# Optimization experiments

Hardware: AMD Instinct MI355X
Metric: run time of the kernel (lower is better)

## Reference

```python
import jax, jax.numpy as jnp
import numpy as np

DIM = 2048
N_HEADS = 16
HEAD_DIM = DIM // N_HEADS
ROPE_BASE = 10000.0


def _rope_cos_sin(seq_len, head_dim, dtype):
    inv_freq = 1.0 / (ROPE_BASE ** (jnp.arange(0, head_dim, 2, dtype=jnp.float32) / head_dim))
    t = jnp.arange(seq_len, dtype=jnp.float32)
    freqs = jnp.einsum('s,d->sd', t, inv_freq)          # (S, hd/2)
    emb = jnp.concatenate([freqs, freqs], axis=-1)       # (S, hd)
    return jnp.cos(emb).astype(dtype), jnp.sin(emb).astype(dtype)


def _rotate_half(x):
    x1, x2 = jnp.split(x, 2, axis=-1)
    return jnp.concatenate([-x2, x1], axis=-1)


def _apply_rope(x, cos, sin):
    # x: (B, H, S, hd); cos/sin: (S, hd)
    return x * cos[None, None] + _rotate_half(x) * sin[None, None]


def setup_inputs() -> dict:
    key = jax.random.key(0)
    ks = jax.random.split(key, 5)
    B, S = 2, 2048
    scale = 1.0 / np.sqrt(DIM)
    return {
        'x': jax.random.normal(ks[0], (B, S, DIM), dtype=jnp.float32),
        'Wq': jax.random.normal(ks[1], (DIM, DIM), dtype=jnp.float32) * scale,
        'Wk': jax.random.normal(ks[2], (DIM, DIM), dtype=jnp.float32) * scale,
        'Wv': jax.random.normal(ks[3], (DIM, DIM), dtype=jnp.float32) * scale,
        'Wo': jax.random.normal(ks[4], (DIM, DIM), dtype=jnp.float32) * scale,
    }


def reference(x, Wq, Wk, Wv, Wo):
    B, S, _ = x.shape
    scale = HEAD_DIM ** -0.5

    def proj(W):
        # torch Linear: x @ W.T ; reshape to (B, H, S, hd)
        return (x @ W.T).reshape(B, S, N_HEADS, HEAD_DIM).transpose(0, 2, 1, 3)

    q, k, v = proj(Wq), proj(Wk), proj(Wv)
    cos, sin = _rope_cos_sin(S, HEAD_DIM, x.dtype)
    q = _apply_rope(q, cos, sin)
    k = _apply_rope(k, cos, sin)

    scores = jnp.einsum('bhqd,bhkd->bhqk', q, k) * scale  # (B,H,S,S)
    causal = jnp.triu(jnp.ones((S, S), dtype=bool), k=1)
    scores = jnp.where(causal[None, None], -jnp.inf, scores)
    attn = jax.nn.softmax(scores.astype(jnp.float32), axis=-1).astype(q.dtype)
    out = jnp.einsum('bhqk,bhkd->bhqd', attn, v)          # (B,H,S,hd)
    out = out.transpose(0, 2, 1, 3).reshape(B, S, DIM)
    return out @ Wo.T
```

## Files before the change

kernel.cpp:

```cpp
#include <hip/hip_runtime.h>


#define SEQ 2048
#define DMODEL 2048
#define NH 16
#define HD 128

typedef __attribute__((ext_vector_type(8))) short bf16x8;
typedef __attribute__((ext_vector_type(4))) float f32x4;

__device__ __forceinline__ unsigned short f2bf(float f) {
  unsigned int u = __float_as_uint(f);
  u += 0x7fffu + ((u >> 16) & 1u);
  return (unsigned short)(u >> 16);
}

__device__ __forceinline__ void g2l16(const void* g, void* l) {
  __builtin_amdgcn_global_load_lds((const __attribute__((address_space(1))) void*)g,
                                   (__attribute__((address_space(3))) void*)l,
                                   16, 0, 0);
}

__device__ __forceinline__ f32x4 mfma16(bf16x8 a, bf16x8 b, f32x4 c) {
  return __builtin_amdgcn_mfma_f32_16x16x32_bf16(a, b, c, 0, 0, 0);
}

template <int CTRL>
__device__ __forceinline__ float dpp_ror(float v) {
  return __int_as_float(__builtin_amdgcn_mov_dpp(__float_as_int(v), CTRL, 0xf, 0xf, false));
}
__device__ __forceinline__ float red_max16(float v) {
  v = fmaxf(v, dpp_ror<0x128>(v));
  v = fmaxf(v, dpp_ror<0x124>(v));
  v = fmaxf(v, dpp_ror<0x122>(v));
  v = fmaxf(v, dpp_ror<0x121>(v));
  return v;
}
__device__ __forceinline__ float red_sum16(float v) {
  v += dpp_ror<0x128>(v);
  v += dpp_ror<0x124>(v);
  v += dpp_ror<0x122>(v);
  v += dpp_ror<0x121>(v);
  return v;
}

__global__ __launch_bounds__(256) void cvt_all(const float* __restrict__ x,
                                               const float* __restrict__ wq,
                                               const float* __restrict__ wk,
                                               const float* __restrict__ wv,
                                               const float* __restrict__ wo,
                                               unsigned short* __restrict__ dst0,
                                               float2* __restrict__ rtab) {
  const int b = blockIdx.x;
  if (b >= 24576) {
    const int idx = (b - 24576) * 256 + threadIdx.x;
    const int s = idx >> 6, d = idx & 63;
    float sn, cs;
    sincosf((float)s * exp2f(-0.20762050593046f * (float)d), &sn, &cs);
    rtab[idx] = make_float2(cs, sn);
    return;
  }
  const float* src;
  unsigned short* dst;
  int idx, r = -1;
  if (b < 8192) {
    src = x; dst = dst0; idx = b * 256 + threadIdx.x;
  } else {
    r = (b - 8192) >> 12;
    src = (r == 0) ? wq : (r == 1) ? wk : (r == 2) ? wv : wo;
    dst = dst0 + (size_t)2 * SEQ * DMODEL + (size_t)r * DMODEL * DMODEL;
    idx = ((b - 8192) & 4095) * 256 + threadIdx.x;
  }
  const float4 v = ((const float4*)src)[idx];
  ushort4 o;
  o.x = f2bf(v.x); o.y = f2bf(v.y); o.z = f2bf(v.z); o.w = f2bf(v.w);
  int widx = idx;
  if (r == 0 || r == 1) {
    const int row = idx >> 9, col = idx & 511;
    const int o_ = row & 127;
    const int e = (((o_ >> 4) & 3) << 5) | (((o_ >> 6) & 1) << 4) | (o_ & 15);
    widx = (((row & ~127) | e) << 9) | col;
  }
  ((ushort4*)dst)[widx] = o;
}

template <int MODE>
__global__ __launch_bounds__(512, 2) void gemm_pipe(
    const unsigned short* __restrict__ A,
    const unsigned short* __restrict__ B,
    unsigned short* __restrict__ obf,
    float* __restrict__ of32,
    const float2* __restrict__ rtab) {
  constexpr int BN = (MODE == 0) ? 192 : 128;
  constexpr int NTW = BN / 32;
  constexpr int TILE = (256 + BN) * 64;
  constexpr int NU = 32 + BN / 8;
  constexpr int UPW = NU / 8;
  __shared__ unsigned short lds[2 * TILE];
  const int nb = blockIdx.x, mb = blockIdx.y;
  const int M0 = mb * 256;
  const int t = threadIdx.x;
  const int w = t >> 6, lane = t & 63, l15 = lane & 15, quad = lane >> 4;
  const int g = lane >> 3, j = lane & 7;
  const int wm = w >> 1, wn = w & 1;

  const unsigned short* Abase = A + (size_t)M0 * DMODEL;
  const unsigned short* Bbase = B + (size_t)nb * BN * DMODEL;

  f32x4 acc[4][NTW] = {};

  auto stage = [&](int buf, int k0, int i0, int i1) {
#pragma unroll
    for (int i = i0; i < i1; ++i) {
      const int u = w * UPW + i;
      if (u < 32) {
        g2l16(Abase + (size_t)(u * 8 + g) * DMODEL + k0 + ((j ^ g) << 3),
              &lds[buf * TILE + u * 512]);
      } else {
        g2l16(Bbase + (size_t)((u - 32) * 8 + g) * DMODEL + k0 + ((j ^ g) << 3),
              &lds[buf * TILE + 16384 + (u - 32) * 512]);
      }
    }
  };

  auto comp = [&](int buf, int kc) {
    const int c = kc * 4 + quad;
    const unsigned short* As_ = &lds[buf * TILE];
    const unsigned short* Bs_ = &lds[buf * TILE + 16384];
    bf16x8 af[4], bv[NTW];
#pragma unroll
    for (int mt = 0; mt < 4; ++mt) {
      const int m = wm * 64 + mt * 16 + l15;
      af[mt] = *(const bf16x8*)&As_[m * 64 + ((c ^ (m & 7)) << 3)];
    }
#pragma unroll
    for (int nt = 0; nt < NTW; ++nt) {
      const int n = wn * (BN / 2) + nt * 16 + l15;
      bv[nt] = *(const bf16x8*)&Bs_[n * 64 + ((c ^ (n & 7)) << 3)];
    }
#pragma unroll
    for (int nt = 0; nt < NTW; ++nt)
#pragma unroll
      for (int mt = 0; mt < 4; ++mt)
        acc[mt][nt] = mfma16(af[mt], bv[nt], acc[mt][nt]);
  };

  stage(0, 0, 0, UPW);
  asm volatile("s_waitcnt vmcnt(0)\n\ts_barrier" ::: "memory");

  int buf = 0;
  for (int tt = 0; tt < 32; ++tt) {
    const bool ps = (tt < 31);
    if (ps) stage(buf ^ 1, tt * 64 + 64, 0, UPW / 2);
    comp(buf, 0);
    if (ps) stage(buf ^ 1, tt * 64 + 64, UPW / 2, UPW);
    comp(buf, 1);
    if (ps) {
      asm volatile("s_waitcnt vmcnt(0)\n\ts_barrier" ::: "memory");
      buf ^= 1;
    }
  }

  if (MODE == 0) {
    const size_t NX = (size_t)2 * SEQ * DMODEL;
#pragma unroll
    for (int pp = 0; pp < NTW / 2; ++pp) {
      const int colb = nb * BN + wn * (BN / 2) + pp * 32;
      const int z = colb >> 11;
      const int zc = colb & 2047;
      const int h = zc >> 7;
      const int e0 = zc & 127;
      if (z < 2) {
        const float qscale = (z == 0) ? 0.1275174356f : 1.0f;
        unsigned short* O = obf + (size_t)z * NX;
        const int rt = (e0 >> 5) * 16 + l15;
#pragma unroll
        for (int mt = 0; mt < 4; ++mt)
#pragma unroll
          for (int reg = 0; reg < 4; ++reg) {
            const int m = M0 + wm * 64 + mt * 16 + quad * 4 + reg;
            const int bb = m >> 11, s = m & 2047;
            unsigned short* ob = O + ((size_t)(bb * NH + h) * SEQ + s) * HD;
            const float2 cs = rtab[s * 64 + rt];
            const float x1 = acc[mt][2 * pp][reg], x2 = acc[mt][2 * pp + 1][reg];
            ob[e0 + l15] = f2bf((x1 * cs.x - x2 * cs.y) * qscale);
            ob[e0 + 16 + l15] = f2bf((x2 * cs.x + x1 * cs.y) * qscale);
          }
      } else {
        unsigned short* Vb0 = obf + 2 * NX + (size_t)h * HD * SEQ;
#pragma unroll
        for (int q2 = 0; q2 < 2; ++q2) {
          const int d = e0 + q2 * 16 + l15;
#pragma unroll
          for (int mt = 0; mt < 4; ++mt)
#pragma unroll
            for (int reg = 0; reg < 4; ++reg) {
              const int m = M0 + wm * 64 + mt * 16 + quad * 4 + reg;
              const int bb = m >> 11, s = m & 2047;
              const int spos = (s & ~63) |
                               ((mt >> 1) * 32 + quad * 8 + reg * 2 + (mt & 1));
              unsigned short* ob = Vb0 + (size_t)bb * NH * HD * SEQ;
              ob[(size_t)d * SEQ + spos] = f2bf(acc[mt][2 * pp + q2][reg]);
            }
        }
      }
    }
  } else {
#pragma unroll
    for (int mt = 0; mt < 4; ++mt)
#pragma unroll
      for (int reg = 0; reg < 4; ++reg) {
        const int m = M0 + wm * 64 + mt * 16 + quad * 4 + reg;
#pragma unroll
        for (int nt = 0; nt < NTW; ++nt)
          of32[(size_t)m * DMODEL + nb * BN + wn * (BN / 2) + nt * 16 + l15] =
              acc[mt][nt][reg];
      }
  }
}

__global__ __launch_bounds__(512, 4) void attn_kernel(const unsigned short* __restrict__ Q,
                                                      const unsigned short* __restrict__ K,
                                                      const unsigned short* __restrict__ Vt,
                                                      unsigned short* __restrict__ Oa) {
  __shared__ unsigned short Ks[2][64 * 128];
  __shared__ unsigned short Vs[2][128 * 64];
  __shared__ unsigned short Ps[8][1024];
  const int gid = blockIdx.x;
  const int bh = gid & 31;
  const int qt = 15 - (gid >> 5);
  const unsigned short* Qb = Q + (size_t)bh * SEQ * HD;
  const unsigned short* Kb = K + (size_t)bh * SEQ * HD;
  const unsigned short* Vb = Vt + (size_t)bh * HD * SEQ;
  const int t = threadIdx.x;
  const int w = t >> 6, lane = t & 63, l15 = lane & 15, quad = lane >> 4;
  const int b = bh >> 4, h = bh & 15;

  auto stage = [&](int sb, int kt) {
    const unsigned short* Kt = Kb + (size_t)(kt * 64) * HD;
    const unsigned short* Vtk = Vb + kt * 64;
#pragma unroll
    for (int i = 0; i < 2; ++i) {
      const int u = i * 512 + t;
      const int key = u >> 4, cs = u & 15;
      g2l16(Kt + (size_t)key * HD + ((cs ^ (key & 7)) << 3),
            &Ks[sb][(i * 512 + w * 64) * 8]);
    }
#pragma unroll
    for (int i = 0; i < 2; ++i) {
      const int u = i * 512 + t;
      const int d = u >> 3, cs = u & 7;
      g2l16(Vtk + (size_t)d * SEQ + ((cs ^ (d & 7)) << 3),
            &Vs[sb][(i * 512 + w * 64) * 8]);
    }
  };

  bf16x8 qf[4];
#pragma unroll
  for (int ch = 0; ch < 4; ++ch)
    qf[ch] = *(const bf16x8*)(Qb + (size_t)(qt * 128 + w * 16 + l15) * HD +
                              ch * 32 + quad * 8);

  f32x4 o[8] = {};
  float mrow[4], lrow[4];
#pragma unroll
  for (int reg = 0; reg < 4; ++reg) { mrow[reg] = -1e30f; lrow[reg] = 0.f; }

  const int ktmax = 2 * qt + 1;
  stage(0, 0);
  asm volatile("s_waitcnt vmcnt(0)\n\ts_barrier" ::: "memory");
  int buf = 0;

  for (int kt = 0; kt <= ktmax; ++kt) {
    if (kt < ktmax) stage(buf ^ 1, kt + 1);

    const int ntm_raw = (qt * 128 + w * 16 + 15 - kt * 64) >> 4;
    const int ntm = ntm_raw > 3 ? 3 : ntm_raw;
    if (ntm >= 0) {
      f32x4 s[4] = {};
      __builtin_amdgcn_s_setprio(1);
#pragma unroll
      for (int ch = 0; ch < 4; ++ch) {
        const int c = ch * 4 + quad;
#pragma unroll
        for (int nt = 0; nt < 4; ++nt) {
          if (nt <= ntm) {
            const int n = nt * 16 + l15;
            const bf16x8 bv = *(const bf16x8*)&Ks[buf][n * 128 + ((c ^ (n & 7)) << 3)];
            s[nt] = mfma16(qf[ch], bv, s[nt]);
          }
        }
      }
      __builtin_amdgcn_s_setprio(0);

      if (kt >= 2 * qt) {
#pragma unroll
        for (int nt = 0; nt < 4; ++nt)
#pragma unroll
          for (int reg = 0; reg < 4; ++reg) {
            const int rr = qt * 128 + w * 16 + quad * 4 + reg;
            const int cc = kt * 64 + nt * 16 + l15;
            if (cc > rr) s[nt][reg] = -1e30f;
          }
      }

#pragma unroll
      for (int reg = 0; reg < 4; ++reg) {
        float vmax = fmaxf(fmaxf(s[0][reg], s[1][reg]), fmaxf(s[2][reg], s[3][reg]));
        vmax = red_max16(vmax);
        const float mo = mrow[reg];
        float mn = mo;
        if (!__all(vmax <= mo + 8.0f)) {
          mn = fmaxf(mo, vmax);
          const float alpha = exp2f(mo - mn);
          mrow[reg] = mn;
          lrow[reg] *= alpha;
#pragma unroll
          for (int nt = 0; nt < 8; ++nt) o[nt][reg] *= alpha;
        }
        float rs = 0.f;
#pragma unroll
        for (int nt = 0; nt < 4; ++nt) {
          const float p_ = exp2f(s[nt][reg] - mn);
          s[nt][reg] = p_;
          rs += p_;
        }
        rs = red_sum16(rs);
        lrow[reg] += rs;
      }

      unsigned short* Pw = Ps[w];
#pragma unroll
      for (int np = 0; np < 2; ++np)
#pragma unroll
        for (int reg = 0; reg < 4; ++reg) {
          unsigned int u;
          asm("v_cvt_pk_bf16_f32 %0, %1, %2"
              : "=v"(u)
              : "v"(s[np * 2][reg]), "v"(s[np * 2 + 1][reg]));
          const int r = quad * 4 + reg;
          const int ph = ((np ^ (quad & 1)) * 4 + (l15 >> 2) + r) & 7;
          *(unsigned int*)&Pw[r * 64 + ph * 8 + (l15 & 3) * 2] = u;
        }
      asm volatile("" ::: "memory");

      const int ch2max = (ntm >= 2) ? 1 : 0;
      __builtin_amdgcn_s_setprio(1);
#pragma unroll
      for (int ch2 = 0; ch2 < 2; ++ch2) {
        if (ch2 <= ch2max) {
          const int pnp = ch2 ^ ((l15 >> 2) & 1);
          const int ph = (pnp * 4 + quad + l15) & 7;
          const bf16x8 pa = *(const bf16x8*)&Pw[l15 * 64 + ph * 8];
          const int c = ch2 * 4 + quad;
#pragma unroll
          for (int nt = 0; nt < 8; ++nt) {
            const int d = nt * 16 + l15;
            const bf16x8 vv = *(const bf16x8*)&Vs[buf][d * 64 + ((c ^ (d & 7)) << 3)];
            o[nt] = mfma16(pa, vv, o[nt]);
          }
        }
      }
      __builtin_amdgcn_s_setprio(0);
    }

    asm volatile("s_waitcnt vmcnt(0)\n\ts_barrier" ::: "memory");
    buf ^= 1;
  }

#pragma unroll
  for (int reg = 0; reg < 4; ++reg) {
    const int sq = qt * 128 + w * 16 + quad * 4 + reg;
    const float inv_l = 1.0f / lrow[reg];
    unsigned short* ob = Oa + (size_t)(b * SEQ + sq) * DMODEL + h * HD;
#pragma unroll
    for (int nt = 0; nt < 8; ++nt) ob[nt * 16 + l15] = f2bf(o[nt][reg] * inv_l);
  }
}

extern "C" void kernel_launch(void* const* d_in, const int* in_sizes, int n_in,
                              void* d_out, int out_size, void* d_ws, size_t ws_size,
                              hipStream_t stream) {
  const float* x = (const float*)d_in[0];
  const float* Wq = (const float*)d_in[1];
  const float* Wk = (const float*)d_in[2];
  const float* Wv = (const float*)d_in[3];
  const float* Wo = (const float*)d_in[4];
  float* out = (float*)d_out;

  const size_t NX = (size_t)2 * SEQ * DMODEL;
  const size_t NW = (size_t)DMODEL * DMODEL;
  unsigned short* ws = (unsigned short*)d_ws;
  unsigned short* xb = ws;
  unsigned short* wqb = xb + NX;
  unsigned short* wkb = wqb + NW;
  unsigned short* wvb = wkb + NW;
  unsigned short* wob = wvb + NW;
  unsigned short* qb = wob + NW;
  unsigned short* kb = qb + NX;
  unsigned short* vb = kb + NX;
  unsigned short* ab = vb + NX;
  float2* rtab = (float2*)(ab + NX);

  cvt_all<<<25088, 256, 0, stream>>>(x, Wq, Wk, Wv, Wo, ws, rtab);
  gemm_pipe<0><<<dim3(32, 16), 512, 0, stream>>>(xb, wqb, qb, nullptr, rtab);
  attn_kernel<<<512, 512, 0, stream>>>(qb, kb, vb, ab);
  gemm_pipe<1><<<dim3(16, 16), 512, 0, stream>>>(ab, wob, nullptr, out, nullptr);
}
```

Baseline: 362.7 us.

## Shrink attention tiles to 64 queries x 32 keys with balanced causal scheduling

The attention kernel now uses 256-thread blocks that each handle 64 query rows, with 32-key K/V tiles instead of 64, and launches twice as many blocks. Query tiles are assigned in a zig-zag order across four rounds so the causal workload is spread more evenly. Staging pointers are precomputed and advanced each step, and the P and V LDS swizzles are redesigned for the 32-wide tile. The cost is more online-softmax rescale and barrier steps per unit of work, and less reuse of each K/V tile.

```diff
diff --git a/kernel.cpp b/kernel.cpp
--- a/kernel.cpp
+++ b/kernel.cpp
@@ -219,46 +219,48 @@
   }
 }
 
-__global__ __launch_bounds__(512, 4) void attn_kernel(const unsigned short* __restrict__ Q,
+__global__ __launch_bounds__(256, 4) void attn_kernel(const unsigned short* __restrict__ Q,
                                                       const unsigned short* __restrict__ K,
                                                       const unsigned short* __restrict__ Vt,
                                                       unsigned short* __restrict__ Oa) {
-  __shared__ unsigned short Ks[2][64 * 128];
-  __shared__ unsigned short Vs[2][128 * 64];
-  __shared__ unsigned short Ps[8][1024];
+  __shared__ unsigned short Ks[2][32 * 128];
+  __shared__ unsigned short Vs[2][128 * 32];
+  __shared__ unsigned short Ps[4][512];
   const int gid = blockIdx.x;
-  const int bh = gid & 31;
-  const int qt = 15 - (gid >> 5);
+  const int r = gid >> 8, c = gid & 255;
+  const int bh = c & 31, u = c >> 5;
+  const int qt = (r == 0) ? 31 - u : (r == 1) ? u : (r == 2) ? 23 - u : 8 + u;
   const unsigned short* Qb = Q + (size_t)bh * SEQ * HD;
-  const unsigned short* Kb = K + (size_t)bh * SEQ * HD;
-  const unsigned short* Vb = Vt + (size_t)bh * HD * SEQ;
   const int t = threadIdx.x;
   const int w = t >> 6, lane = t & 63, l15 = lane & 15, quad = lane >> 4;
   const int b = bh >> 4, h = bh & 15;
 
-  auto stage = [&](int sb, int kt) {
-    const unsigned short* Kt = Kb + (size_t)(kt * 64) * HD;
-    const unsigned short* Vtk = Vb + kt * 64;
-#pragma unroll
-    for (int i = 0; i < 2; ++i) {
-      const int u = i * 512 + t;
-      const int key = u >> 4, cs = u & 15;
-      g2l16(Kt + (size_t)key * HD + ((cs ^ (key & 7)) << 3),
-            &Ks[sb][(i * 512 + w * 64) * 8]);
-    }
-#pragma unroll
-    for (int i = 0; i < 2; ++i) {
-      const int u = i * 512 + t;
-      const int d = u >> 3, cs = u & 7;
-      g2l16(Vtk + (size_t)d * SEQ + ((cs ^ (d & 7)) << 3),
-            &Vs[sb][(i * 512 + w * 64) * 8]);
-    }
+  const int uk0 = t, uk1 = 256 + t;
+  const int k0key = uk0 >> 4, k0cs = uk0 & 15;
+  const int k1key = uk1 >> 4, k1cs = uk1 & 15;
+  const unsigned short* kp0 = K + (size_t)bh * SEQ * HD +
+                              (size_t)k0key * HD + (((k0cs ^ (k0key & 7)) & 15) << 3);
+  const unsigned short* kp1 = K + (size_t)bh * SEQ * HD +
+                              (size_t)k1key * HD + (((k1cs ^ (k1key & 7)) & 15) << 3);
+  const int v0d = uk0 >> 2, v0cs = uk0 & 3;
+  const int v1d = uk1 >> 2, v1cs = uk1 & 3;
+  const unsigned short* vp0 = Vt + (size_t)bh * HD * SEQ +
+                              (size_t)v0d * SEQ + ((v0cs ^ ((v0d >> 1) & 3)) << 3);
+  const unsigned short* vp1 = Vt + (size_t)bh * HD * SEQ +
+                              (size_t)v1d * SEQ + ((v1cs ^ ((v1d >> 1) & 3)) << 3);
+
+  auto stage = [&](int sb) {
+    g2l16(kp0, &Ks[sb][(w * 64) * 8]);
+    g2l16(kp1, &Ks[sb][(256 + w * 64) * 8]);
+    g2l16(vp0, &Vs[sb][(w * 64) * 8]);
+    g2l16(vp1, &Vs[sb][(256 + w * 64) * 8]);
+    kp0 += 32 * HD; kp1 += 32 * HD; vp0 += 32; vp1 += 32;
   };
 
   bf16x8 qf[4];
 #pragma unroll
   for (int ch = 0; ch < 4; ++ch)
-    qf[ch] = *(const bf16x8*)(Qb + (size_t)(qt * 128 + w * 16 + l15) * HD +
+    qf[ch] = *(const bf16x8*)(Qb + (size_t)(qt * 64 + w * 16 + l15) * HD +
                               ch * 32 + quad * 8);
 
   f32x4 o[8] = {};
@@ -267,46 +269,46 @@
   for (int reg = 0; reg < 4; ++reg) { mrow[reg] = -1e30f; lrow[reg] = 0.f; }
 
   const int ktmax = 2 * qt + 1;
-  stage(0, 0);
+  stage(0);
   asm volatile("s_waitcnt vmcnt(0)\n\ts_barrier" ::: "memory");
   int buf = 0;
 
   for (int kt = 0; kt <= ktmax; ++kt) {
-    if (kt < ktmax) stage(buf ^ 1, kt + 1);
-
-    const int ntm_raw = (qt * 128 + w * 16 + 15 - kt * 64) >> 4;
-    const int ntm = ntm_raw > 3 ? 3 : ntm_raw;
+    if (kt < ktmax) stage(buf ^ 1);
+
+    const bool dz = (kt >= 2 * qt);
+    const int ntm = dz ? ((qt * 64 + w * 16 + 15 - kt * 32) >> 4) : 1;
     if (ntm >= 0) {
-      f32x4 s[4] = {};
+      f32x4 s[2] = {};
       __builtin_amdgcn_s_setprio(1);
 #pragma unroll
       for (int ch = 0; ch < 4; ++ch) {
-        const int c = ch * 4 + quad;
-#pragma unroll
-        for (int nt = 0; nt < 4; ++nt) {
+        const int cc = ch * 4 + quad;
+#pragma unroll
+        for (int nt = 0; nt < 2; ++nt) {
           if (nt <= ntm) {
             const int n = nt * 16 + l15;
-            const bf16x8 bv = *(const bf16x8*)&Ks[buf][n * 128 + ((c ^ (n & 7)) << 3)];
+            const bf16x8 bv = *(const bf16x8*)&Ks[buf][n * 128 + ((cc ^ (n & 7)) << 3)];
             s[nt] = mfma16(qf[ch], bv, s[nt]);
           }
         }
       }
       __builtin_amdgcn_s_setprio(0);
 
-      if (kt >= 2 * qt) {
-#pragma unroll
-        for (int nt = 0; nt < 4; ++nt)
+      if (dz) {
+#pragma unroll
+        for (int nt = 0; nt < 2; ++nt)
 #pragma unroll
           for (int reg = 0; reg < 4; ++reg) {
-            const int rr = qt * 128 + w * 16 + quad * 4 + reg;
-            const int cc = kt * 64 + nt * 16 + l15;
+            const int rr = qt * 64 + w * 16 + quad * 4 + reg;
+            const int cc = kt * 32 + nt * 16 + l15;
             if (cc > rr) s[nt][reg] = -1e30f;
           }
       }
 
 #pragma unroll
       for (int reg = 0; reg < 4; ++reg) {
-        float vmax = fmaxf(fmaxf(s[0][reg], s[1][reg]), fmaxf(s[2][reg], s[3][reg]));
+        float vmax = fmaxf(s[0][reg], s[1][reg]);
         vmax = red_max16(vmax);
         const float mo = mrow[reg];
         float mn = mo;
@@ -320,7 +322,7 @@
         }
         float rs = 0.f;
 #pragma unroll
-        for (int nt = 0; nt < 4; ++nt) {
+        for (int nt = 0; nt < 2; ++nt) {
           const float p_ = exp2f(s[nt][reg] - mn);
           s[nt][reg] = p_;
           rs += p_;
@@ -329,37 +331,24 @@
         lrow[reg] += rs;
       }
 
-      unsigned short* Pw = Ps[w];
-#pragma unroll
-      for (int np = 0; np < 2; ++np)
-#pragma unroll
-        for (int reg = 0; reg < 4; ++reg) {
-          unsigned int u;
-          asm("v_cvt_pk_bf16_f32 %0, %1, %2"
-              : "=v"(u)
-              : "v"(s[np * 2][reg]), "v"(s[np * 2 + 1][reg]));
-          const int r = quad * 4 + reg;
-          const int ph = ((np ^ (quad & 1)) * 4 + (l15 >> 2) + r) & 7;
-          *(unsigned int*)&Pw[r * 64 + ph * 8 + (l15 & 3) * 2] = u;
-        }
+      unsigned int* Pw32 = (unsigned int*)Ps[w];
+#pragma unroll
+      for (int reg = 0; reg < 4; ++reg) {
+        unsigned int pu;
+        asm("v_cvt_pk_bf16_f32 %0, %1, %2"
+            : "=v"(pu)
+            : "v"(s[0][reg]), "v"(s[1][reg]));
+        Pw32[(quad * 4 + reg) * 16 + (((l15 >> 2) ^ reg) << 2) + (l15 & 3)] = pu;
+      }
       asm volatile("" ::: "memory");
 
-      const int ch2max = (ntm >= 2) ? 1 : 0;
+      const bf16x8 pa = *(const bf16x8*)&Ps[w][l15 * 32 + ((quad ^ (l15 & 3)) << 3)];
       __builtin_amdgcn_s_setprio(1);
 #pragma unroll
-      for (int ch2 = 0; ch2 < 2; ++ch2) {
-        if (ch2 <= ch2max) {
-          const int pnp = ch2 ^ ((l15 >> 2) & 1);
-          const int ph = (pnp * 4 + quad + l15) & 7;
-          const bf16x8 pa = *(const bf16x8*)&Pw[l15 * 64 + ph * 8];
-          const int c = ch2 * 4 + quad;
-#pragma unroll
-          for (int nt = 0; nt < 8; ++nt) {
-            const int d = nt * 16 + l15;
-            const bf16x8 vv = *(const bf16x8*)&Vs[buf][d * 64 + ((c ^ (d & 7)) << 3)];
-            o[nt] = mfma16(pa, vv, o[nt]);
-          }
-        }
+      for (int nt = 0; nt < 8; ++nt) {
+        const int d = nt * 16 + l15;
+        const bf16x8 vv = *(const bf16x8*)&Vs[buf][d * 32 + ((quad ^ ((d >> 1) & 3)) << 3)];
+        o[nt] = mfma16(pa, vv, o[nt]);
       }
       __builtin_amdgcn_s_setprio(0);
     }
@@ -370,7 +359,7 @@
 
 #pragma unroll
   for (int reg = 0; reg < 4; ++reg) {
-    const int sq = qt * 128 + w * 16 + quad * 4 + reg;
+    const int sq = qt * 64 + w * 16 + quad * 4 + reg;
     const float inv_l = 1.0f / lrow[reg];
     unsigned short* ob = Oa + (size_t)(b * SEQ + sq) * DMODEL + h * HD;
 #pragma unroll
@@ -404,6 +393,6 @@
 
   cvt_all<<<25088, 256, 0, stream>>>(x, Wq, Wk, Wv, Wo, ws, rtab);
   gemm_pipe<0><<<dim3(32, 16), 512, 0, stream>>>(xb, wqb, qb, nullptr, rtab);
-  attn_kernel<<<512, 512, 0, stream>>>(qb, kb, vb, ab);
+  attn_kernel<<<1024, 256, 0, stream>>>(qb, kb, vb, ab);
   gemm_pipe<1><<<dim3(16, 16), 512, 0, stream>>>(ab, wob, nullptr, out, nullptr);
 }
```

Measured after the change: 372.8 us. 1.03x slower.
